# Kernel tuning notes

Hardware: AMD Instinct MI355X
Metric: run time of the kernel (lower is better)

The kernel has to match this reference:

```python
import jax, jax.numpy as jnp
import numpy as np

TEMPERATURE = 0.1
NSAMPLE = 32
B, N_PER, M_PER, C_FEAT = 2, 16384, 4096, 64


def setup_inputs() -> dict:
    key = jax.random.key(0)
    ks = jax.random.split(key, 4)
    xyz = jax.random.normal(ks[0], (B * N_PER, 3), jnp.float32)
    new_xyz = jax.random.normal(ks[1], (B * M_PER, 3), jnp.float32)
    new_xyz_r = jax.random.uniform(ks[2], (B * M_PER, 1), jnp.float32, minval=0.5, maxval=1.0)
    features = jax.random.normal(ks[3], (B * N_PER, C_FEAT), jnp.float32)
    xyz_batch_cnt = jnp.full((B,), N_PER, jnp.int32)
    new_xyz_batch_cnt = jnp.full((B,), M_PER, jnp.int32)
    temperature_decay = jnp.ones((1,), jnp.float32)
    return dict(xyz=xyz, xyz_batch_cnt=xyz_batch_cnt, new_xyz=new_xyz,
                new_xyz_r=new_xyz_r, new_xyz_batch_cnt=new_xyz_batch_cnt,
                features=features, temperature_decay=temperature_decay)


def _ball_query(xyz_b, new_xyz_b, r_b, nsample):
    # xyz_b: (B,N,3), new_xyz_b: (B,M,3), r_b: (B,M)
    # Returns idx (B,M,nsample) int32 (batch-local point indices, first-in-order
    # within the ball, remaining slots filled with first hit, 0 if empty) and
    # empty mask (B,M) bool. Mirrors the CUDA ball_query_deform kernel.
    N = xyz_b.shape[1]
    d2 = jnp.sum((new_xyz_b[:, :, None, :] - xyz_b[:, None, :, :]) ** 2, axis=-1)  # (B,M,N)
    within = d2 < (r_b ** 2)[..., None]
    # key = point index if within radius else N; top_k of -key gives the first
    # nsample in-ball indices in ascending index order.
    key = jnp.where(within, jnp.arange(N, dtype=jnp.int32), jnp.int32(N))
    neg_vals, _ = jax.lax.top_k(-key, nsample)
    cand = -neg_vals  # (B,M,nsample)
    cnt = within.sum(axis=-1)  # (B,M)
    slot_valid = jnp.arange(nsample) < cnt[..., None]
    idx = jnp.where(slot_valid, cand, cand[..., :1])  # pad with first found index
    empty = cnt == 0
    idx = jnp.where(empty[..., None], 0, idx)
    return idx.astype(jnp.int32), empty


def reference(xyz, xyz_batch_cnt, new_xyz, new_xyz_r, new_xyz_batch_cnt, features, temperature_decay):
    b = xyz_batch_cnt.shape[0]
    n = xyz.shape[0] // b
    m = new_xyz.shape[0] // b
    c = features.shape[1]
    real_t = TEMPERATURE * temperature_decay[0]
    explore_r = new_xyz_r + real_t * 5.0  # (M_tot, 1)

    xyz_b = xyz.reshape(b, n, 3)
    nxyz_b = new_xyz.reshape(b, m, 3)
    idx_b, empty_b = _ball_query(xyz_b, nxyz_b, explore_r.reshape(b, m), NSAMPLE)

    gather = jax.vmap(lambda pts, i: pts[i])  # per-batch gather

    grouped_xyz = gather(xyz_b, idx_b)                 # (B,M,ns,3)
    grouped_xyz = grouped_xyz - nxyz_b[:, :, None, :]  # center
    grouped_xyz = jnp.where(empty_b[:, :, None, None], 0.0, grouped_xyz)
    grouped_xyz = grouped_xyz.reshape(b * m, NSAMPLE, 3).transpose(0, 2, 1)  # (M_tot,3,ns)

    dist_xyz = jnp.sqrt(jnp.sum(grouped_xyz * grouped_xyz, axis=1))  # (M_tot,ns)
    weights = 1.0 - jax.nn.sigmoid((dist_xyz - new_xyz_r) / real_t)  # (M_tot,ns)

    feat_b = features.reshape(b, n, c)
    grouped_feat = gather(feat_b, idx_b)  # (B,M,ns,C)
    grouped_feat = jnp.where(empty_b[:, :, None, None], 0.0, grouped_feat)
    grouped_feat = grouped_feat.reshape(b * m, NSAMPLE, c).transpose(0, 2, 1)  # (M_tot,C,ns)

    new_features = jnp.concatenate([grouped_xyz, grouped_feat], axis=1)  # (M_tot,3+C,ns)
    idx = idx_b.reshape(b * m, NSAMPLE)
    return new_features, weights, idx
```

## Files before the change

### kernel.cpp

```cpp
#include <hip/hip_runtime.h>
#include <math.h>

#define NS 32
#define WPB 4
#define SCAN0 2048
#define TSTRIDE 36

__global__ __launch_bounds__(256) void qgd_scanA(
    const float* __restrict__ xyz, const float* __restrict__ new_xyz,
    const float* __restrict__ new_xyz_r, const float* __restrict__ tdec,
    int* __restrict__ idx_out,
    int* __restrict__ counter, int* __restrict__ list,
    int N_per, int M_per, int M_tot)
{
#pragma clang fp contract(off)
    const int lane = threadIdx.x & 63;
    const int wv   = threadIdx.x >> 6;
    const int m    = blockIdx.x * WPB + wv;
    if (m >= M_tot) return;

    const int bb = m / M_per;
    const float* xb = xyz + (size_t)bb * N_per * 3;
    const float qx = new_xyz[(size_t)m * 3 + 0];
    const float qy = new_xyz[(size_t)m * 3 + 1];
    const float qz = new_xyz[(size_t)m * 3 + 2];
    const float r_orig = new_xyz_r[m];
    const float real_t = 0.1f * tdec[0];
    const float er  = r_orig + real_t * 5.0f;
    const float er2 = er * er;
    const unsigned long long lt = (1ull << lane) - 1ull;

    const int scan0 = (SCAN0 < N_per) ? SCAN0 : N_per;
    int cnt = 0;
    for (int base = 0; base < scan0; base += 256) {
        float d2k[4];
        #pragma unroll
        for (int k = 0; k < 4; ++k) {
            int p = base + k * 64 + lane;
            int pc = (p < N_per) ? p : (N_per - 1);
            const float* pp = xb + (size_t)pc * 3;
            float dx = pp[0] - qx, dy = pp[1] - qy, dz = pp[2] - qz;
            float d2 = dx * dx;
            d2 = d2 + dy * dy;
            d2 = d2 + dz * dz;
            d2k[k] = (p < N_per) ? d2 : 1e30f;
        }
        #pragma unroll
        for (int k = 0; k < 4; ++k) {
            bool hit = d2k[k] < er2;
            unsigned long long msk = __ballot(hit);
            if (hit) {
                int slot = cnt + (int)__popcll(msk & lt);
                if (slot < NS) idx_out[(size_t)m * NS + slot] = base + k * 64 + lane;
            }
            cnt += (int)__popcll(msk);
        }
        if (cnt >= NS) break;
    }
    if (cnt < NS && lane == 0) {
        int pos = atomicAdd(counter, 1);
        list[pos] = m;
    }
}

__global__ __launch_bounds__(256) void qgd_scanB(
    const float* __restrict__ xyz, const float* __restrict__ new_xyz,
    const float* __restrict__ new_xyz_r, const float* __restrict__ tdec,
    int* __restrict__ idx_out,
    const int* __restrict__ counter, const int* __restrict__ list,
    int N_per, int M_per)
{
#pragma clang fp contract(off)
    __shared__ int sH[WPB][NS];
    __shared__ int sC[WPB];

    const int lane = threadIdx.x & 63;
    const int wv   = threadIdx.x >> 6;
    const int nstrag = *counter;
    const unsigned long long lt = (1ull << lane) - 1ull;

    for (int it = blockIdx.x; it < nstrag; it += gridDim.x) {
        const int m  = list[it];
        const int bb = m / M_per;
        const float* xb = xyz + (size_t)bb * N_per * 3;
        const float qx = new_xyz[(size_t)m * 3 + 0];
        const float qy = new_xyz[(size_t)m * 3 + 1];
        const float qz = new_xyz[(size_t)m * 3 + 2];
        const float r_orig = new_xyz_r[m];
        const float real_t = 0.1f * tdec[0];
        const float er  = r_orig + real_t * 5.0f;
        const float er2 = er * er;

        const int rb = (int)(((long long)N_per * wv) / WPB);
        const int re = (int)(((long long)N_per * (wv + 1)) / WPB);

        int cnt = 0;
        for (int base = rb; base < re; base += 256) {
            float d2k[4];
            #pragma unroll
            for (int k = 0; k < 4; ++k) {
                int p = base + k * 64 + lane;
                int pc = (p < re) ? p : (re - 1);
                const float* pp = xb + (size_t)pc * 3;
                float dx = pp[0] - qx, dy = pp[1] - qy, dz = pp[2] - qz;
                float d2 = dx * dx;
                d2 = d2 + dy * dy;
                d2 = d2 + dz * dz;
                d2k[k] = (p < re) ? d2 : 1e30f;
            }
            #pragma unroll
            for (int k = 0; k < 4; ++k) {
                bool hit = d2k[k] < er2;
                unsigned long long msk = __ballot(hit);
                if (hit) {
                    int slot = cnt + (int)__popcll(msk & lt);
                    if (slot < NS) sH[wv][slot] = base + k * 64 + lane;
                }
                cnt += (int)__popcll(msk);
            }
            if (cnt >= NS) break;
        }
        if (lane == 0) sC[wv] = (cnt < NS) ? cnt : NS;
        __syncthreads();

        if (threadIdx.x < NS) {
            const int j  = threadIdx.x;
            const int c0 = sC[0], c1 = sC[1], c2 = sC[2], c3 = sC[3];
            const int o1 = c0, o2 = c0 + c1, o3 = o2 + c2;
            const int tot = o3 + c3;
            int v = 0;
            if (j < tot) {
                if      (j >= o3) v = sH[3][j - o3];
                else if (j >= o2) v = sH[2][j - o2];
                else if (j >= o1) v = sH[1][j - o1];
                else              v = sH[0][j];
            }
            int first = -1;
            if      (c0 > 0) first = sH[0][0];
            else if (c1 > 0) first = sH[1][0];
            else if (c2 > 0) first = sH[2][0];
            else if (c3 > 0) first = sH[3][0];
            int outv;
            if (tot == 0)      outv = (j == 0) ? -1 : 0;
            else if (j < tot)  outv = v;
            else               outv = first;
            idx_out[(size_t)m * NS + j] = outv;
        }
        __syncthreads();
    }
}

__global__ __launch_bounds__(256) void qgd_writeC(
    const float* __restrict__ xyz, const float* __restrict__ new_xyz,
    const float* __restrict__ new_xyz_r, const float* __restrict__ features,
    const float* __restrict__ tdec, float* __restrict__ out,
    int N_per, int M_per, int C, int M_tot)
{
#pragma clang fp contract(off)
    __shared__ __align__(16) float sBuf[WPB * 32 * TSTRIDE];
    __shared__ int sIdx[WPB][NS];

    const int lane = threadIdx.x & 63;
    const int wv   = threadIdx.x >> 6;
    const int m    = blockIdx.x * WPB + wv;
    const bool active = (m < M_tot);

    float* wout = out + (size_t)M_tot * (3 + C) * NS;
    float* iout = wout + (size_t)M_tot * NS;
    int*   iint = (int*)iout;

    if (active && lane < NS) sIdx[wv][lane] = iint[(size_t)m * NS + lane];
    __syncthreads();

    if (!active) return;

    const bool empty = (sIdx[wv][0] < 0);
    const int  bb    = m / M_per;
    const float* xb  = xyz + (size_t)bb * N_per * 3;
    const int    j   = lane & 31;
    const size_t nf_base = (size_t)m * (3 + C) * NS;

    if (lane < NS) {
        const float qx = new_xyz[(size_t)m * 3 + 0];
        const float qy = new_xyz[(size_t)m * 3 + 1];
        const float qz = new_xyz[(size_t)m * 3 + 2];
        const float r_orig = new_xyz_r[m];
        const float real_t = 0.1f * tdec[0];
        const int pj = empty ? 0 : sIdx[wv][j];
        float gx = 0.f, gy = 0.f, gz = 0.f;
        if (!empty) {
            gx = xb[(size_t)pj * 3 + 0] - qx;
            gy = xb[(size_t)pj * 3 + 1] - qy;
            gz = xb[(size_t)pj * 3 + 2] - qz;
        }
        float d2 = gx * gx;
        d2 = d2 + gy * gy;
        d2 = d2 + gz * gz;
        float dist = sqrtf(d2);
        float wt = 1.0f / (1.0f + expf((dist - r_orig) / real_t));
        out[nf_base + 0 * NS + j] = gx;
        out[nf_base + 1 * NS + j] = gy;
        out[nf_base + 2 * NS + j] = gz;
        wout[(size_t)m * NS + j] = wt;
        iout[(size_t)m * NS + j] = (float)pj;
    }

    float* sT = sBuf + wv * (32 * TSTRIDE);
    const float* fb = features + (size_t)bb * N_per * C;

    int c0 = 0;
    for (; c0 + 32 <= C; c0 += 32) {
        {
            const int k  = lane & 7;
            const int f4 = 4 * (k & 3);
            #pragma unroll
            for (int t = 0; t < 4; ++t) {
                const int r  = 8 * t + (lane >> 3);
                const int pj = empty ? 0 : sIdx[wv][r];
                float4 v = make_float4(0.f, 0.f, 0.f, 0.f);
                if (!empty) v = *(const float4*)(fb + (size_t)pj * C + c0 + 4 * k);
                const int rs = r ^ f4;
                sT[(4 * k + 0) * TSTRIDE + rs] = v.x;
                sT[(4 * k + 1) * TSTRIDE + rs] = v.y;
                sT[(4 * k + 2) * TSTRIDE + rs] = v.z;
                sT[(4 * k + 3) * TSTRIDE + rs] = v.w;
            }
        }
        __syncthreads();
        {
            const int jg = lane & 7;
            #pragma unroll
            for (int s2 = 0; s2 < 4; ++s2) {
                const int ch = 8 * s2 + (lane >> 3);
                const int jb = (4 * jg) ^ (4 * ((ch >> 2) & 3));
                float4 w = *(const float4*)&sT[ch * TSTRIDE + jb];
                *(float4*)&out[nf_base + (size_t)(3 + c0 + ch) * NS + 4 * jg] = w;
            }
        }
        __syncthreads();
    }
    if (c0 < C) {
        const int h  = lane >> 5;
        const int pj = empty ? 0 : sIdx[wv][j];
        const float* frow = fb + (size_t)pj * C;
        for (int c = c0 + h; c < C; c += 2) {
            float v = empty ? 0.f : frow[c];
            out[nf_base + (size_t)(3 + c) * NS + j] = v;
        }
    }
}

extern "C" void kernel_launch(void* const* d_in, const int* in_sizes, int n_in,
                              void* d_out, int out_size, void* d_ws, size_t ws_size,
                              hipStream_t stream) {
    const float* xyz       = (const float*)d_in[0];
    const float* new_xyz   = (const float*)d_in[2];
    const float* new_xyz_r = (const float*)d_in[3];
    const float* features  = (const float*)d_in[5];
    const float* tdec      = (const float*)d_in[6];

    const int B     = in_sizes[1];
    const int N_tot = in_sizes[0] / 3;
    const int M_tot = in_sizes[2] / 3;
    const int C     = in_sizes[5] / N_tot;
    const int N_per = N_tot / B;
    const int M_per = M_tot / B;

    float* out  = (float*)d_out;
    int*   iint = (int*)(out + (size_t)M_tot * (3 + C) * NS + (size_t)M_tot * NS);
    int*   counter = (int*)d_ws;
    int*   list    = (int*)d_ws + 4;

    hipMemsetAsync(counter, 0, sizeof(int), stream);

    const int blocksA = (M_tot + WPB - 1) / WPB;
    qgd_scanA<<<blocksA, 256, 0, stream>>>(xyz, new_xyz, new_xyz_r, tdec,
                                           iint, counter, list,
                                           N_per, M_per, M_tot);
    qgd_scanB<<<512, 256, 0, stream>>>(xyz, new_xyz, new_xyz_r, tdec,
                                       iint, counter, list, N_per, M_per);
    const int blocksC = (M_tot + WPB - 1) / WPB;
    qgd_writeC<<<blocksC, 256, 0, stream>>>(xyz, new_xyz, new_xyz_r, features,
                                            tdec, out, N_per, M_per, C, M_tot);
}
```

Baseline: 124.2 us.

## Fuse output write into scan kernels, drop separate gather pass

Queries that fill all 32 slots within the first scan window now write their grouped xyz, features, weights and indices directly from the scan kernel, using shared memory for the index list. Straggler queries get the same output write at the end of the second-pass kernel. This removes the third kernel launch and the round-trip of indices through global memory. In exchange the first kernel uses more shared memory and registers, which may reduce occupancy, and in the straggler kernel only one wave does the write while the other waves wait.

```diff
diff --git a/kernel.cpp b/kernel.cpp
--- a/kernel.cpp
+++ b/kernel.cpp
@@ -6,14 +6,92 @@
 #define SCAN0 2048
 #define TSTRIDE 36
 
-__global__ __launch_bounds__(256) void qgd_scanA(
+__device__ __forceinline__ void write_query(
+    int m, int bb, bool empty, int lane,
+    const int* sIdxW, float* sT,
     const float* __restrict__ xyz, const float* __restrict__ new_xyz,
-    const float* __restrict__ new_xyz_r, const float* __restrict__ tdec,
-    int* __restrict__ idx_out,
-    int* __restrict__ counter, int* __restrict__ list,
-    int N_per, int M_per, int M_tot)
+    const float* __restrict__ new_xyz_r, const float* __restrict__ features,
+    float real_t, float* __restrict__ out, int N_per, int C, int M_tot)
 {
 #pragma clang fp contract(off)
+    const float* xb = xyz + (size_t)bb * N_per * 3;
+    const int    j  = lane & 31;
+    const size_t nf_base = (size_t)m * (3 + C) * NS;
+    float* wout = out + (size_t)M_tot * (3 + C) * NS;
+    float* iout = wout + (size_t)M_tot * NS;
+
+    if (lane < NS) {
+        const float qx = new_xyz[(size_t)m * 3 + 0];
+        const float qy = new_xyz[(size_t)m * 3 + 1];
+        const float qz = new_xyz[(size_t)m * 3 + 2];
+        const float r_orig = new_xyz_r[m];
+        const int pj = empty ? 0 : sIdxW[j];
+        float gx = 0.f, gy = 0.f, gz = 0.f;
+        if (!empty) {
+            gx = xb[(size_t)pj * 3 + 0] - qx;
+            gy = xb[(size_t)pj * 3 + 1] - qy;
+            gz = xb[(size_t)pj * 3 + 2] - qz;
+        }
+        float d2 = gx * gx;
+        d2 = d2 + gy * gy;
+        d2 = d2 + gz * gz;
+        float dist = sqrtf(d2);
+        float wt = 1.0f / (1.0f + expf((dist - r_orig) / real_t));
+        out[nf_base + 0 * NS + j] = gx;
+        out[nf_base + 1 * NS + j] = gy;
+        out[nf_base + 2 * NS + j] = gz;
+        wout[(size_t)m * NS + j] = wt;
+        iout[(size_t)m * NS + j] = (float)pj;
+    }
+
+    const float* fb = features + (size_t)bb * N_per * C;
+    int c0 = 0;
+    for (; c0 + 32 <= C; c0 += 32) {
+        const int k  = lane & 7;
+        const int f4 = 4 * (k & 3);
+        #pragma unroll
+        for (int t = 0; t < 4; ++t) {
+            const int r  = 8 * t + (lane >> 3);
+            const int pj = empty ? 0 : sIdxW[r];
+            float4 v = make_float4(0.f, 0.f, 0.f, 0.f);
+            if (!empty) v = *(const float4*)(fb + (size_t)pj * C + c0 + 4 * k);
+            const int rs = r ^ f4;
+            sT[(4 * k + 0) * TSTRIDE + rs] = v.x;
+            sT[(4 * k + 1) * TSTRIDE + rs] = v.y;
+            sT[(4 * k + 2) * TSTRIDE + rs] = v.z;
+            sT[(4 * k + 3) * TSTRIDE + rs] = v.w;
+        }
+        const int jg = lane & 7;
+        #pragma unroll
+        for (int s2 = 0; s2 < 4; ++s2) {
+            const int ch = 8 * s2 + (lane >> 3);
+            const int jb = (4 * jg) ^ (4 * ((ch >> 2) & 3));
+            float4 w = *(const float4*)&sT[ch * TSTRIDE + jb];
+            *(float4*)&out[nf_base + (size_t)(3 + c0 + ch) * NS + 4 * jg] = w;
+        }
+    }
+    if (c0 < C) {
+        const int h  = lane >> 5;
+        const int pj = empty ? 0 : sIdxW[j];
+        const float* frow = fb + (size_t)pj * C;
+        for (int c = c0 + h; c < C; c += 2) {
+            float v = empty ? 0.f : frow[c];
+            out[nf_base + (size_t)(3 + c) * NS + j] = v;
+        }
+    }
+}
+
+__global__ __launch_bounds__(256) void qgd_AC(
+    const float* __restrict__ xyz, const float* __restrict__ new_xyz,
+    const float* __restrict__ new_xyz_r, const float* __restrict__ features,
+    const float* __restrict__ tdec, float* __restrict__ out,
+    int* __restrict__ counter, int* __restrict__ list,
+    int N_per, int M_per, int C, int M_tot)
+{
+#pragma clang fp contract(off)
+    __shared__ __align__(16) float sBuf[WPB * 32 * TSTRIDE];
+    __shared__ int sIdx[WPB][NS];
+
     const int lane = threadIdx.x & 63;
     const int wv   = threadIdx.x >> 6;
     const int m    = blockIdx.x * WPB + wv;
@@ -24,9 +102,8 @@
     const float qx = new_xyz[(size_t)m * 3 + 0];
     const float qy = new_xyz[(size_t)m * 3 + 1];
     const float qz = new_xyz[(size_t)m * 3 + 2];
-    const float r_orig = new_xyz_r[m];
     const float real_t = 0.1f * tdec[0];
-    const float er  = r_orig + real_t * 5.0f;
+    const float er  = new_xyz_r[m] + real_t * 5.0f;
     const float er2 = er * er;
     const unsigned long long lt = (1ull << lane) - 1ull;
 
@@ -51,33 +128,43 @@
             unsigned long long msk = __ballot(hit);
             if (hit) {
                 int slot = cnt + (int)__popcll(msk & lt);
-                if (slot < NS) idx_out[(size_t)m * NS + slot] = base + k * 64 + lane;
+                if (slot < NS) sIdx[wv][slot] = base + k * 64 + lane;
             }
             cnt += (int)__popcll(msk);
         }
         if (cnt >= NS) break;
     }
-    if (cnt < NS && lane == 0) {
+
+    if (cnt >= NS) {
+        write_query(m, bb, false, lane, sIdx[wv],
+                    sBuf + wv * (32 * TSTRIDE),
+                    xyz, new_xyz, new_xyz_r, features, real_t, out,
+                    N_per, C, M_tot);
+    } else if (lane == 0) {
         int pos = atomicAdd(counter, 1);
         list[pos] = m;
     }
 }
 
-__global__ __launch_bounds__(256) void qgd_scanB(
+__global__ __launch_bounds__(256) void qgd_B(
     const float* __restrict__ xyz, const float* __restrict__ new_xyz,
-    const float* __restrict__ new_xyz_r, const float* __restrict__ tdec,
-    int* __restrict__ idx_out,
+    const float* __restrict__ new_xyz_r, const float* __restrict__ features,
+    const float* __restrict__ tdec, float* __restrict__ out,
     const int* __restrict__ counter, const int* __restrict__ list,
-    int N_per, int M_per)
+    int N_per, int M_per, int C, int M_tot)
 {
 #pragma clang fp contract(off)
     __shared__ int sH[WPB][NS];
     __shared__ int sC[WPB];
+    __shared__ int sM[NS];
+    __shared__ int sTot;
+    __shared__ __align__(16) float sT[32 * TSTRIDE];
 
     const int lane = threadIdx.x & 63;
     const int wv   = threadIdx.x >> 6;
     const int nstrag = *counter;
     const unsigned long long lt = (1ull << lane) - 1ull;
+    const float real_t = 0.1f * tdec[0];
 
     for (int it = blockIdx.x; it < nstrag; it += gridDim.x) {
         const int m  = list[it];
@@ -86,9 +173,7 @@
         const float qx = new_xyz[(size_t)m * 3 + 0];
         const float qy = new_xyz[(size_t)m * 3 + 1];
         const float qz = new_xyz[(size_t)m * 3 + 2];
-        const float r_orig = new_xyz_r[m];
-        const float real_t = 0.1f * tdec[0];
-        const float er  = r_orig + real_t * 5.0f;
+        const float er  = new_xyz_r[m] + real_t * 5.0f;
         const float er2 = er * er;
 
         const int rb = (int)(((long long)N_per * wv) / WPB);
@@ -135,118 +220,22 @@
                 else if (j >= o1) v = sH[1][j - o1];
                 else              v = sH[0][j];
             }
-            int first = -1;
+            int first = 0;
             if      (c0 > 0) first = sH[0][0];
             else if (c1 > 0) first = sH[1][0];
             else if (c2 > 0) first = sH[2][0];
             else if (c3 > 0) first = sH[3][0];
-            int outv;
-            if (tot == 0)      outv = (j == 0) ? -1 : 0;
-            else if (j < tot)  outv = v;
-            else               outv = first;
-            idx_out[(size_t)m * NS + j] = outv;
+            sM[j] = (tot == 0) ? 0 : ((j < tot) ? v : first);
+            if (j == 0) sTot = tot;
         }
         __syncthreads();
-    }
-}
-
-__global__ __launch_bounds__(256) void qgd_writeC(
-    const float* __restrict__ xyz, const float* __restrict__ new_xyz,
-    const float* __restrict__ new_xyz_r, const float* __restrict__ features,
-    const float* __restrict__ tdec, float* __restrict__ out,
-    int N_per, int M_per, int C, int M_tot)
-{
-#pragma clang fp contract(off)
-    __shared__ __align__(16) float sBuf[WPB * 32 * TSTRIDE];
-    __shared__ int sIdx[WPB][NS];
-
-    const int lane = threadIdx.x & 63;
-    const int wv   = threadIdx.x >> 6;
-    const int m    = blockIdx.x * WPB + wv;
-    const bool active = (m < M_tot);
-
-    float* wout = out + (size_t)M_tot * (3 + C) * NS;
-    float* iout = wout + (size_t)M_tot * NS;
-    int*   iint = (int*)iout;
-
-    if (active && lane < NS) sIdx[wv][lane] = iint[(size_t)m * NS + lane];
-    __syncthreads();
-
-    if (!active) return;
-
-    const bool empty = (sIdx[wv][0] < 0);
-    const int  bb    = m / M_per;
-    const float* xb  = xyz + (size_t)bb * N_per * 3;
-    const int    j   = lane & 31;
-    const size_t nf_base = (size_t)m * (3 + C) * NS;
-
-    if (lane < NS) {
-        const float qx = new_xyz[(size_t)m * 3 + 0];
-        const float qy = new_xyz[(size_t)m * 3 + 1];
-        const float qz = new_xyz[(size_t)m * 3 + 2];
-        const float r_orig = new_xyz_r[m];
-        const float real_t = 0.1f * tdec[0];
-        const int pj = empty ? 0 : sIdx[wv][j];
-        float gx = 0.f, gy = 0.f, gz = 0.f;
-        if (!empty) {
-            gx = xb[(size_t)pj * 3 + 0] - qx;
-            gy = xb[(size_t)pj * 3 + 1] - qy;
-            gz = xb[(size_t)pj * 3 + 2] - qz;
-        }
-        float d2 = gx * gx;
-        d2 = d2 + gy * gy;
-        d2 = d2 + gz * gz;
-        float dist = sqrtf(d2);
-        float wt = 1.0f / (1.0f + expf((dist - r_orig) / real_t));
-        out[nf_base + 0 * NS + j] = gx;
-        out[nf_base + 1 * NS + j] = gy;
-        out[nf_base + 2 * NS + j] = gz;
-        wout[(size_t)m * NS + j] = wt;
-        iout[(size_t)m * NS + j] = (float)pj;
-    }
-
-    float* sT = sBuf + wv * (32 * TSTRIDE);
-    const float* fb = features + (size_t)bb * N_per * C;
-
-    int c0 = 0;
-    for (; c0 + 32 <= C; c0 += 32) {
-        {
-            const int k  = lane & 7;
-            const int f4 = 4 * (k & 3);
-            #pragma unroll
-            for (int t = 0; t < 4; ++t) {
-                const int r  = 8 * t + (lane >> 3);
-                const int pj = empty ? 0 : sIdx[wv][r];
-                float4 v = make_float4(0.f, 0.f, 0.f, 0.f);
-                if (!empty) v = *(const float4*)(fb + (size_t)pj * C + c0 + 4 * k);
-                const int rs = r ^ f4;
-                sT[(4 * k + 0) * TSTRIDE + rs] = v.x;
-                sT[(4 * k + 1) * TSTRIDE + rs] = v.y;
-                sT[(4 * k + 2) * TSTRIDE + rs] = v.z;
-                sT[(4 * k + 3) * TSTRIDE + rs] = v.w;
-            }
+
+        if (wv == 0) {
+            write_query(m, bb, (sTot == 0), lane, sM, sT,
+                        xyz, new_xyz, new_xyz_r, features, real_t, out,
+                        N_per, C, M_tot);
         }
         __syncthreads();
-        {
-            const int jg = lane & 7;
-            #pragma unroll
-            for (int s2 = 0; s2 < 4; ++s2) {
-                const int ch = 8 * s2 + (lane >> 3);
-                const int jb = (4 * jg) ^ (4 * ((ch >> 2) & 3));
-                float4 w = *(const float4*)&sT[ch * TSTRIDE + jb];
-                *(float4*)&out[nf_base + (size_t)(3 + c0 + ch) * NS + 4 * jg] = w;
-            }
-        }
-        __syncthreads();
-    }
-    if (c0 < C) {
-        const int h  = lane >> 5;
-        const int pj = empty ? 0 : sIdx[wv][j];
-        const float* frow = fb + (size_t)pj * C;
-        for (int c = c0 + h; c < C; c += 2) {
-            float v = empty ? 0.f : frow[c];
-            out[nf_base + (size_t)(3 + c) * NS + j] = v;
-        }
     }
 }
 
@@ -266,20 +255,17 @@
     const int N_per = N_tot / B;
     const int M_per = M_tot / B;
 
-    float* out  = (float*)d_out;
-    int*   iint = (int*)(out + (size_t)M_tot * (3 + C) * NS + (size_t)M_tot * NS);
+    float* out     = (float*)d_out;
     int*   counter = (int*)d_ws;
     int*   list    = (int*)d_ws + 4;
 
     hipMemsetAsync(counter, 0, sizeof(int), stream);
 
     const int blocksA = (M_tot + WPB - 1) / WPB;
-    qgd_scanA<<<blocksA, 256, 0, stream>>>(xyz, new_xyz, new_xyz_r, tdec,
-                                           iint, counter, list,
-                                           N_per, M_per, M_tot);
-    qgd_scanB<<<512, 256, 0, stream>>>(xyz, new_xyz, new_xyz_r, tdec,
-                                       iint, counter, list, N_per, M_per);
-    const int blocksC = (M_tot + WPB - 1) / WPB;
-    qgd_writeC<<<blocksC, 256, 0, stream>>>(xyz, new_xyz, new_xyz_r, features,
-                                            tdec, out, N_per, M_per, C, M_tot);
-}
+    qgd_AC<<<blocksA, 256, 0, stream>>>(xyz, new_xyz, new_xyz_r, features,
+                                        tdec, out, counter, list,
+                                        N_per, M_per, C, M_tot);
+    qgd_B<<<512, 256, 0, stream>>>(xyz, new_xyz, new_xyz_r, features,
+                                   tdec, out, counter, list,
+                                   N_per, M_per, C, M_tot);
+}
```

Result: faster. 119.2 us (-4.0%).
